# Kernel tuning notes

Hardware: AMD Instinct MI355X
Metric: run time of the kernel (lower is better)

Reference implementation:

```python
import jax, jax.numpy as jnp
import numpy as np

N, E, F_IN, H, K = 100000, 1600000, 256, 128, 5


def setup_inputs() -> dict:
    key = jax.random.key(0)
    ks = jax.random.split(key, 24)

    def rn(k, shape, scale=0.05):
        return jax.random.normal(k, shape, dtype=jnp.float32) * scale

    inp = {
        "x": rn(ks[0], (N, F_IN), 1.0),
        "edge_index": jax.random.randint(ks[1], (2, E), 0, N, dtype=jnp.int64),
        "edge_attr": jax.random.uniform(ks[2], (N, K), dtype=jnp.float32),
        "pre_W": rn(ks[3], (F_IN, H)),
        "pre_b": jnp.zeros((H,), jnp.float32),
        "c1_Ws": rn(ks[4], (H, H)),
        "c1_Wn": rn(ks[5], (H, H)),
        "c1_b": jnp.zeros((H,), jnp.float32),
        "c2_Ws": rn(ks[6], (H, H)),
        "c2_Wn": rn(ks[7], (H, H)),
        "c2_b": jnp.zeros((H,), jnp.float32),
        "nodepost_W": rn(ks[8], (H, H)),
        "nodepost_b": jnp.zeros((H,), jnp.float32),
        "d_W0": rn(ks[9], (K, H)),
        "d_b0": jnp.zeros((H,), jnp.float32),
        "d_W1": rn(ks[10], (H, H)),
        "d_b1": jnp.zeros((H,), jnp.float32),
        "d_W2": rn(ks[11], (H, H)),
        "d_b2": jnp.zeros((H,), jnp.float32),
        "d_W3": rn(ks[12], (H, H)),
        "d_b3": jnp.zeros((H,), jnp.float32),
        "final_W": rn(ks[13], (2 * H, 1)),
        "final_b": jnp.zeros((1,), jnp.float32),
    }
    return inp


def _mean_agg(h, src, dst, n):
    # scatter-mean of source features onto destination nodes
    s = jax.ops.segment_sum(h[src], dst, num_segments=n)  # [N, H]
    deg = jax.ops.segment_sum(jnp.ones_like(dst, dtype=h.dtype), dst, num_segments=n)
    return s / jnp.maximum(deg, 1.0)[:, None]


def reference(x, edge_index, edge_attr, pre_W, pre_b,
              c1_Ws, c1_Wn, c1_b, c2_Ws, c2_Wn, c2_b,
              nodepost_W, nodepost_b,
              d_W0, d_b0, d_W1, d_b1, d_W2, d_b2, d_W3, d_b3,
              final_W, final_b):
    n = x.shape[0]
    src, dst = edge_index[0], edge_index[1]

    # --- feat path: NodeAttributeAggregator ---
    h = x @ pre_W + pre_b                                   # pre_process_mlp
    agg = _mean_agg(h, src, dst, n)
    h = jax.nn.relu(h @ c1_Ws + agg @ c1_Wn + c1_b)          # layer1 conv + act
    agg = _mean_agg(h, src, dst, n)
    h = jax.nn.relu(h @ c2_Ws + agg @ c2_Wn + c2_b)          # layer2 conv + act
    feat_out = h @ nodepost_W + nodepost_b                   # post_process_mlp

    # --- dist path: EdgeAttributeAggregator (MLP over edge attrs) ---
    e = edge_attr.reshape(-1, K)
    y = jax.nn.relu(e @ d_W0 + d_b0)
    y = jax.nn.relu(y @ d_W1 + d_b1)
    y = jax.nn.relu(y @ d_W2 + d_b2)
    dist_out = y @ d_W3 + d_b3

    # --- merge 'cat' + final MLP + squeeze + sigmoid ---
    z = jnp.concatenate([feat_out, dist_out], axis=1)        # [N, 2H]
    out = (z @ final_W + final_b).squeeze(1)                  # [N]
    return jax.nn.sigmoid(out)
```

## Files before the change

kernel.cpp:

```cpp
#include <hip/hip_runtime.h>

#define HF 128
#define CAP 64
#define PSHIFT 17
#define BUCKET_BLOCKS 2048

typedef __attribute__((ext_vector_type(8))) short s16x8;
typedef __attribute__((ext_vector_type(4))) float f32x4;
typedef __attribute__((ext_vector_type(2))) float f32x2;

__device__ __forceinline__ unsigned short f2bf(float f) {
    unsigned u = __float_as_uint(f);
    return (unsigned short)((u + 0x7fff + ((u >> 16) & 1)) >> 16);
}
__device__ __forceinline__ float bflo(unsigned u) { return __uint_as_float(u << 16); }
__device__ __forceinline__ float bfhi(unsigned u) { return __uint_as_float(u & 0xffff0000u); }

#if __has_builtin(__builtin_amdgcn_cvt_pk_fp8_f32) && __has_builtin(__builtin_amdgcn_cvt_pk_f32_fp8)
#define FP8_HW 1
#else
#define FP8_HW 0
#endif

__device__ __forceinline__ unsigned char f2fp8(float f) {
#if FP8_HW
    int v = __builtin_amdgcn_cvt_pk_fp8_f32(f, f, 0, false);
    return (unsigned char)(v & 0xff);
#else
    unsigned u = __float_as_uint(f);
    unsigned s = (u >> 24) & 0x80;
    float a = fabsf(f);
    if (a > 448.f) a = 448.f;
    if (a < 0.015625f) {
        int q = (int)(a * 512.f + 0.5f);
        return (unsigned char)(s | q);
    }
    unsigned ub = __float_as_uint(a);
    ub += 0x0007ffff + ((ub >> 20) & 1);
    int e8 = (int)(ub >> 23) - 127 + 7;
    if (e8 >= 16) return (unsigned char)(s | 0x7e);
    return (unsigned char)(s | (e8 << 3) | ((ub >> 20) & 7));
#endif
}

__device__ __forceinline__ void fp8acc4(unsigned w, float* acc) {
#if FP8_HW
    f32x2 lo = __builtin_amdgcn_cvt_pk_f32_fp8(w, false);
    f32x2 hi = __builtin_amdgcn_cvt_pk_f32_fp8(w, true);
    acc[0] += lo.x; acc[1] += lo.y; acc[2] += hi.x; acc[3] += hi.y;
#else
    #pragma unroll
    for (int j = 0; j < 4; ++j) {
        unsigned b = (w >> (8 * j)) & 0xff;
        unsigned s = (b >> 7) & 1, e = (b >> 3) & 15, m = b & 7;
        float v = e ? __uint_as_float(((e + 120) << 23) | (m << 20))
                    : (float)m * 0.001953125f;
        acc[j] += s ? -v : v;
    }
#endif
}

__device__ __forceinline__ void repack_one(
    const float* __restrict__ W, short* __restrict__ Wp, int K, int t)
{
    int nkt = K >> 5;
    int lane = t & 63;
    int kt = (t >> 6) % nkt;
    int nt = (t >> 6) / nkt;
    int c = nt * 16 + (lane & 15);
    int kbase = kt * 32 + (lane >> 4) * 8;
    s16x8 v;
    #pragma unroll
    for (int j = 0; j < 8; ++j) v[j] = (short)f2bf(W[(long)(kbase + j) * HF + c]);
    *(s16x8*)(Wp + (long)t * 8) = v;
}

__global__ __launch_bounds__(256) void repack_all(
    const float* __restrict__ preW, const float* __restrict__ c1Ws,
    const float* __restrict__ c1Wn, const float* __restrict__ c2Ws,
    const float* __restrict__ c2Wn, const float* __restrict__ dW1,
    const float* __restrict__ dW2,
    short* preWp, short* c1Wsp, short* c1Wnp, short* c2Wsp, short* c2Wnp,
    short* dW1p, short* dW2p,
    const float* __restrict__ npW, const float* __restrict__ npb,
    const float* __restrict__ dW3, const float* __restrict__ db3,
    const float* __restrict__ fW,  const float* __restrict__ fb,
    float* __restrict__ uvc)
{
    int b = blockIdx.x;
    if (b == 64) {
        int i = threadIdx.x;
        if (i < HF) {
            float u = 0.f, v = 0.f;
            for (int j = 0; j < HF; ++j) {
                u += npW[i * HF + j] * fW[j];
                v += dW3[i * HF + j] * fW[HF + j];
            }
            uvc[i] = u;
            uvc[HF + i] = v;
            if (i == 0) {
                float c = fb[0];
                for (int j = 0; j < HF; ++j) c += npb[j] * fW[j] + db3[j] * fW[HF + j];
                uvc[2 * HF] = c;
            }
        }
        return;
    }
    if (b < 16) { repack_one(preW, preWp, 256, b * 256 + threadIdx.x); return; }
    int m = (b - 16) >> 3, t = ((b - 16) & 7) * 256 + threadIdx.x;
    const float* W; short* Wp;
    switch (m) {
        case 0: W = c1Ws; Wp = c1Wsp; break;
        case 1: W = c1Wn; Wp = c1Wnp; break;
        case 2: W = c2Ws; Wp = c2Wsp; break;
        case 3: W = c2Wn; Wp = c2Wnp; break;
        case 4: W = dW1;  Wp = dW1p;  break;
        default: W = dW2; Wp = dW2p;  break;
    }
    repack_one(W, Wp, HF, t);
}

__global__ __launch_bounds__(256) void bucketx_kernel(
    const int* __restrict__ eidx, long E,
    int* __restrict__ deg, int* __restrict__ bucket, int npass)
{
    const int xcd   = blockIdx.x & 7;
    const int chunk = blockIdx.x >> 3;
    const int nchunks = BUCKET_BLOCKS / 8;
    long per = (E + nchunks - 1) / nchunks;
    per = (per + 3) & ~3L;
    const long e0 = (long)chunk * per;
    const long e1 = (e0 + per < E) ? e0 + per : E;
    if (e0 >= E) return;
    for (int p = 0; p < npass; ++p) {
        for (long e = e0 + (long)threadIdx.x * 4; e + 4 <= e1; e += 1024) {
            int4 d4 = *(const int4*)(eidx + E + e);
            #pragma unroll
            for (int j = 0; j < 4; ++j) {
                int d = (&d4.x)[j];
                if ((d >> PSHIFT) != p || ((d >> 4) & 7) != xcd) continue;
                int s = eidx[e + j];
                int pos = atomicAdd(&deg[d], 1);
                if (pos < CAP) bucket[(long)d * CAP + pos] = s;
            }
        }
        for (long e = (e1 & ~3L) + threadIdx.x; e < e1; e += 256) {
            int d = eidx[E + e];
            if ((d >> PSHIFT) != p || ((d >> 4) & 7) != xcd) continue;
            int s = eidx[e];
            int pos = atomicAdd(&deg[d], 1);
            if (pos < CAP) bucket[(long)d * CAP + pos] = s;
        }
    }
}

__device__ __forceinline__ void agg_tile512(
    const unsigned char* __restrict__ hq, const int* __restrict__ deg,
    const int* __restrict__ bucket, int n, long row0B, int wv, int lane,
    unsigned* lds)
{
    const int g = lane >> 4;
    const int i = lane & 15;
    #pragma unroll
    for (int it = 0; it < 2; ++it) {
        const int rl = wv * 8 + it * 4 + g;
        const long node = row0B + rl;
        float acc[8];
        #pragma unroll
        for (int j = 0; j < 8; ++j) acc[j] = 0.f;
        int dg = 0, m = 0;
        const int* bl = bucket;
        if (node < n) {
            dg = deg[node];
            m = dg < CAP ? dg : CAP;
            bl = bucket + node * CAP;
        }
        int e = 0;
        for (; e + 8 <= m; e += 8) {
            int4 sa = *(const int4*)(bl + e);
            int4 sb = *(const int4*)(bl + e + 4);
            uint2 v0 = *(const uint2*)(hq + (long)sa.x * HF + i * 8);
            uint2 v1 = *(const uint2*)(hq + (long)sa.y * HF + i * 8);
            uint2 v2 = *(const uint2*)(hq + (long)sa.z * HF + i * 8);
            uint2 v3 = *(const uint2*)(hq + (long)sa.w * HF + i * 8);
            uint2 v4 = *(const uint2*)(hq + (long)sb.x * HF + i * 8);
            uint2 v5 = *(const uint2*)(hq + (long)sb.y * HF + i * 8);
            uint2 v6 = *(const uint2*)(hq + (long)sb.z * HF + i * 8);
            uint2 v7 = *(const uint2*)(hq + (long)sb.w * HF + i * 8);
            fp8acc4(v0.x, acc); fp8acc4(v0.y, acc + 4);
            fp8acc4(v1.x, acc); fp8acc4(v1.y, acc + 4);
            fp8acc4(v2.x, acc); fp8acc4(v2.y, acc + 4);
            fp8acc4(v3.x, acc); fp8acc4(v3.y, acc + 4);
            fp8acc4(v4.x, acc); fp8acc4(v4.y, acc + 4);
            fp8acc4(v5.x, acc); fp8acc4(v5.y, acc + 4);
            fp8acc4(v6.x, acc); fp8acc4(v6.y, acc + 4);
            fp8acc4(v7.x, acc); fp8acc4(v7.y, acc + 4);
        }
        for (; e + 4 <= m; e += 4) {
            int4 sa = *(const int4*)(bl + e);
            uint2 v0 = *(const uint2*)(hq + (long)sa.x * HF + i * 8);
            uint2 v1 = *(const uint2*)(hq + (long)sa.y * HF + i * 8);
            uint2 v2 = *(const uint2*)(hq + (long)sa.z * HF + i * 8);
            uint2 v3 = *(const uint2*)(hq + (long)sa.w * HF + i * 8);
            fp8acc4(v0.x, acc); fp8acc4(v0.y, acc + 4);
            fp8acc4(v1.x, acc); fp8acc4(v1.y, acc + 4);
            fp8acc4(v2.x, acc); fp8acc4(v2.y, acc + 4);
            fp8acc4(v3.x, acc); fp8acc4(v3.y, acc + 4);
        }
        for (; e < m; ++e) {
            uint2 v = *(const uint2*)(hq + (long)bl[e] * HF + i * 8);
            fp8acc4(v.x, acc); fp8acc4(v.y, acc + 4);
        }
        const float sc = 1.f / (float)(dg > 1 ? dg : 1);
        uint4 o;
        o.x = (unsigned)f2bf(acc[0] * sc) | ((unsigned)f2bf(acc[1] * sc) << 16);
        o.y = (unsigned)f2bf(acc[2] * sc) | ((unsigned)f2bf(acc[3] * sc) << 16);
        o.z = (unsigned)f2bf(acc[4] * sc) | ((unsigned)f2bf(acc[5] * sc) << 16);
        o.w = (unsigned)f2bf(acc[6] * sc) | ((unsigned)f2bf(acc[7] * sc) << 16);
        *(uint4*)&lds[rl * 64 + ((i ^ (rl & 15)) << 2)] = o;
    }
}

template<int K, bool F32>
__device__ __forceinline__ void gemm_pass_mfma(
    const void* __restrict__ Av, const short* __restrict__ Wp,
    long rA, int lane, f32x4 acc[8])
{
    const int q = lane >> 4;
    constexpr int NKT = K >> 5;
    #pragma unroll
    for (int kt = 0; kt < NKT; ++kt) {
        s16x8 a;
        if (F32) {
            const float* p = (const float*)Av + rA * K + kt * 32 + q * 8;
            float4 f0 = *(const float4*)p;
            float4 f1 = *(const float4*)(p + 4);
            a[0] = (short)f2bf(f0.x); a[1] = (short)f2bf(f0.y);
            a[2] = (short)f2bf(f0.z); a[3] = (short)f2bf(f0.w);
            a[4] = (short)f2bf(f1.x); a[5] = (short)f2bf(f1.y);
            a[6] = (short)f2bf(f1.z); a[7] = (short)f2bf(f1.w);
        } else {
            a = *(const s16x8*)((const unsigned short*)Av + rA * K + kt * 32 + q * 8);
        }
        #pragma unroll
        for (int nt = 0; nt < 8; ++nt) {
            s16x8 b = *(const s16x8*)(Wp + ((long)(nt * NKT + kt) * 64 + lane) * 8);
            acc[nt] = __builtin_amdgcn_mfma_f32_16x16x32_bf16(a, b, acc[nt], 0, 0, 0);
        }
    }
}

__device__ __forceinline__ void gemm_pass_lds(
    const unsigned* lds, int w, int lane, const short* __restrict__ Wp, f32x4 acc[8])
{
    const int q = lane >> 4;
    const int i15 = lane & 15;
    const int rl = w * 16 + i15;
    #pragma unroll
    for (int kt = 0; kt < 4; ++kt) {
        s16x8 a = *(const s16x8*)&lds[rl * 64 + (((kt * 4 + q) ^ i15) << 2)];
        #pragma unroll
        for (int nt = 0; nt < 8; ++nt) {
            s16x8 b = *(const s16x8*)(Wp + ((long)(nt * 4 + kt) * 64 + lane) * 8);
            acc[nt] = __builtin_amdgcn_mfma_f32_16x16x32_bf16(a, b, acc[nt], 0, 0, 0);
        }
    }
}

__device__ void pre_body(int gb, const float* __restrict__ x, const short* __restrict__ preWp,
                         const float* __restrict__ preb, unsigned short* __restrict__ h0,
                         unsigned char* __restrict__ h0q, int n)
{
    const int lane = threadIdx.x & 63;
    const int wv   = threadIdx.x >> 6;
    const long row0 = (long)gb * 64 + wv * 16;

    f32x4 acc[8];
    #pragma unroll
    for (int nt = 0; nt < 8; ++nt)
        #pragma unroll
        for (int i = 0; i < 4; ++i) acc[nt][i] = 0.f;

    long rA = row0 + (lane & 15);
    if (rA > n - 1) rA = n - 1;

    gemm_pass_mfma<256, true>(x, preWp, rA, lane, acc);

    const int cq = lane >> 4;
    #pragma unroll
    for (int nt = 0; nt < 8; ++nt) {
        int col = nt * 16 + (lane & 15);
        float bs = preb[col];
        #pragma unroll
        for (int i = 0; i < 4; ++i) {
            long r = row0 + cq * 4 + i;
            if (r < n) {
                float o = acc[nt][i] + bs;
                h0[r * HF + col] = f2bf(o);
                h0q[r * HF + col] = f2fp8(o);
            }
        }
    }
}

__device__ void disthead_body(int gb,
    const float* __restrict__ ea, const float* __restrict__ W0,
    const float* __restrict__ b0, const short* __restrict__ W1p,
    const float* __restrict__ b1, unsigned short* __restrict__ y1, int n)
{
    const int lane = threadIdx.x & 63;
    const int wv   = threadIdx.x >> 6;
    const long row0 = (long)gb * 64 + wv * 16;
    const int q = lane >> 4;
    long rA = row0 + (lane & 15);
    if (rA > n - 1) rA = n - 1;

    float e0 = ea[rA * 5 + 0], e1 = ea[rA * 5 + 1], e2 = ea[rA * 5 + 2],
          e3 = ea[rA * 5 + 3], e4 = ea[rA * 5 + 4];

    f32x4 acc[8];
    #pragma unroll
    for (int nt = 0; nt < 8; ++nt)
        #pragma unroll
        for (int i = 0; i < 4; ++i) acc[nt][i] = 0.f;

    #pragma unroll
    for (int kt = 0; kt < 4; ++kt) {
        const int c = kt * 32 + q * 8;
        s16x8 a;
        #pragma unroll
        for (int h = 0; h < 2; ++h) {
            float4 w0 = *(const float4*)(W0 + 0 * HF + c + h * 4);
            float4 w1 = *(const float4*)(W0 + 1 * HF + c + h * 4);
            float4 w2 = *(const float4*)(W0 + 2 * HF + c + h * 4);
            float4 w3 = *(const float4*)(W0 + 3 * HF + c + h * 4);
            float4 w4 = *(const float4*)(W0 + 4 * HF + c + h * 4);
            float4 bb = *(const float4*)(b0 + c + h * 4);
            float z0 = fmaxf(bb.x + e0 * w0.x + e1 * w1.x + e2 * w2.x + e3 * w3.x + e4 * w4.x, 0.f);
            float z1 = fmaxf(bb.y + e0 * w0.y + e1 * w1.y + e2 * w2.y + e3 * w3.y + e4 * w4.y, 0.f);
            float z2 = fmaxf(bb.z + e0 * w0.z + e1 * w1.z + e2 * w2.z + e3 * w3.z + e4 * w4.z, 0.f);
            float z3 = fmaxf(bb.w + e0 * w0.w + e1 * w1.w + e2 * w2.w + e3 * w3.w + e4 * w4.w, 0.f);
            a[h * 4 + 0] = (short)f2bf(z0); a[h * 4 + 1] = (short)f2bf(z1);
            a[h * 4 + 2] = (short)f2bf(z2); a[h * 4 + 3] = (short)f2bf(z3);
        }
        #pragma unroll
        for (int nt = 0; nt < 8; ++nt) {
            s16x8 b = *(const s16x8*)(W1p + ((long)(nt * 4 + kt) * 64 + lane) * 8);
            acc[nt] = __builtin_amdgcn_mfma_f32_16x16x32_bf16(a, b, acc[nt], 0, 0, 0);
        }
    }

    const int cq = lane >> 4;
    #pragma unroll
    for (int nt = 0; nt < 8; ++nt) {
        int col = nt * 16 + (lane & 15);
        float bs = b1[col];
        #pragma unroll
        for (int i = 0; i < 4; ++i) {
            long r = row0 + cq * 4 + i;
            if (r < n) y1[r * HF + col] = f2bf(fmaxf(acc[nt][i] + bs, 0.f));
        }
    }
}

__global__ __launch_bounds__(256) void megapd_kernel(
    const float* __restrict__ x, const short* __restrict__ preWp,
    const float* __restrict__ preb, unsigned short* __restrict__ h0,
    unsigned char* __restrict__ h0q,
    const float* __restrict__ ea, const float* __restrict__ W0,
    const float* __restrict__ b0, const short* __restrict__ W1p,
    const float* __restrict__ b1, unsigned short* __restrict__ y1,
    int n, int gemmBlocks)
{
    if (blockIdx.x < gemmBlocks)
        pre_body(blockIdx.x, x, preWp, preb, h0, h0q, n);
    else
        disthead_body(blockIdx.x - gemmBlocks, ea, W0, b0, W1p, b1, y1, n);
}

__global__ __launch_bounds__(512) void c1f_kernel(
    const unsigned short* __restrict__ h0, const unsigned char* __restrict__ h0q,
    const int* __restrict__ deg, const int* __restrict__ bucket,
    const short* __restrict__ Wsp, const short* __restrict__ Wnp,
    const float* __restrict__ bias, unsigned short* __restrict__ out,
    unsigned char* __restrict__ outq, int n)
{
    __shared__ unsigned ldsagg[64 * 64];
    const int lane = threadIdx.x & 63;
    const int wv   = threadIdx.x >> 6;
    const long row0B = (long)blockIdx.x * 64;

    agg_tile512(h0q, deg, bucket, n, row0B, wv, lane, ldsagg);
    __syncthreads();

    if (wv >= 4) return;

    f32x4 acc[8];
    #pragma unroll
    for (int nt = 0; nt < 8; ++nt)
        #pragma unroll
        for (int i = 0; i < 4; ++i) acc[nt][i] = 0.f;

    const long row0 = row0B + wv * 16;
    long rA = row0 + (lane & 15);
    if (rA > n - 1) rA = n - 1;

    gemm_pass_mfma<HF, false>((const void*)h0, Wsp, rA, lane, acc);
    gemm_pass_lds(ldsagg, wv, lane, Wnp, acc);

    const int cq = lane >> 4;
    #pragma unroll
    for (int nt = 0; nt < 8; ++nt) {
        int col = nt * 16 + (lane & 15);
        float bs = bias[col];
        #pragma unroll
        for (int i = 0; i < 4; ++i) {
            long r = row0 + cq * 4 + i;
            if (r < n) {
                float o = fmaxf(acc[nt][i] + bs, 0.f);
                out[r * HF + col] = f2bf(o);
                outq[r * HF + col] = f2fp8(o);
            }
        }
    }
}

__global__ __launch_bounds__(512) void tailf_kernel(
    const unsigned short* __restrict__ h1, const unsigned char* __restrict__ h1q,
    const unsigned short* __restrict__ y1,
    const int* __restrict__ deg, const int* __restrict__ bucket,
    const short* __restrict__ c2Wsp, const short* __restrict__ c2Wnp,
    const short* __restrict__ dW2p,
    const float* __restrict__ c2b, const float* __restrict__ db2,
    const float* __restrict__ uvc, float* __restrict__ out, int n)
{
    __shared__ unsigned ldsagg[64 * 64];
    __shared__ float pp[2][64];
    const int lane = threadIdx.x & 63;
    const int wv   = threadIdx.x >> 6;
    const long row0B = (long)blockIdx.x * 64;

    agg_tile512(h1q, deg, bucket, n, row0B, wv, lane, ldsagg);
    __syncthreads();

    const int w = wv & 3;
    const long row0 = row0B + w * 16;
    long rA = row0 + (lane & 15);
    if (rA > n - 1) rA = n - 1;
    const int cq = lane >> 4;
    float part[4] = {0.f, 0.f, 0.f, 0.f};

    f32x4 acc[8];
    #pragma unroll
    for (int nt = 0; nt < 8; ++nt)
        #pragma unroll
        for (int i = 0; i < 4; ++i) acc[nt][i] = 0.f;

    if (wv < 4) {
        gemm_pass_mfma<HF, false>((const void*)h1, c2Wsp, rA, lane, acc);
        gemm_pass_lds(ldsagg, w, lane, c2Wnp, acc);
        #pragma unroll
        for (int nt = 0; nt < 8; ++nt) {
            int col = nt * 16 + (lane & 15);
            float bh = c2b[col], uu = uvc[col];
            #pragma unroll
            for (int i = 0; i < 4; ++i)
                part[i] += fmaxf(acc[nt][i] + bh, 0.f) * uu;
        }
    } else {
        gemm_pass_mfma<HF, false>((const void*)y1, dW2p, rA, lane, acc);
        #pragma unroll
        for (int nt = 0; nt < 8; ++nt) {
            int col = nt * 16 + (lane & 15);
            float by = db2[col], vv = uvc[HF + col];
            #pragma unroll
            for (int i = 0; i < 4; ++i)
                part[i] += fmaxf(acc[nt][i] + by, 0.f) * vv;
        }
    }

    #pragma unroll
    for (int i = 0; i < 4; ++i) {
        float s = part[i];
        s += __shfl_xor(s, 1, 64);
        s += __shfl_xor(s, 2, 64);
        s += __shfl_xor(s, 4, 64);
        s += __shfl_xor(s, 8, 64);
        part[i] = s;
    }
    if ((lane & 15) == 0) {
        #pragma unroll
        for (int i = 0; i < 4; ++i)
            pp[wv >> 2][w * 16 + cq * 4 + i] = part[i];
    }
    __syncthreads();

    if (threadIdx.x < 64) {
        long r = row0B + threadIdx.x;
        if (r < n) {
            float s = pp[0][threadIdx.x] + pp[1][threadIdx.x] + uvc[2 * HF];
            out[r] = 1.f / (1.f + expf(-s));
        }
    }
}

extern "C" void kernel_launch(void* const* d_in, const int* in_sizes, int n_in,
                              void* d_out, int out_size, void* d_ws, size_t ws_size,
                              hipStream_t stream)
{
    const float* x      = (const float*)d_in[0];
    const int*   eidx   = (const int*)  d_in[1];
    const float* eattr  = (const float*)d_in[2];
    const float* pre_W  = (const float*)d_in[3];
    const float* pre_b  = (const float*)d_in[4];
    const float* c1_Ws  = (const float*)d_in[5];
    const float* c1_Wn  = (const float*)d_in[6];
    const float* c1_b   = (const float*)d_in[7];
    const float* c2_Ws  = (const float*)d_in[8];
    const float* c2_Wn  = (const float*)d_in[9];
    const float* c2_b   = (const float*)d_in[10];
    const float* npW    = (const float*)d_in[11];
    const float* npb    = (const float*)d_in[12];
    const float* dW0    = (const float*)d_in[13];
    const float* db0    = (const float*)d_in[14];
    const float* dW1    = (const float*)d_in[15];
    const float* db1    = (const float*)d_in[16];
    const float* dW2    = (const float*)d_in[17];
    const float* db2    = (const float*)d_in[18];
    const float* dW3    = (const float*)d_in[19];
    const float* db3    = (const float*)d_in[20];
    const float* fW     = (const float*)d_in[21];
    const float* fb     = (const float*)d_in[22];

    const int  n = in_sizes[0] / 256;
    const long E = in_sizes[1] / 2;

    char* ws = (char*)d_ws;
    size_t off = 0;
    auto alloc = [&](size_t bytes) -> void* {
        void* p = ws + off;
        off += (bytes + 255) & ~(size_t)255;
        return p;
    };
    unsigned short* B0 = (unsigned short*)alloc((size_t)n * HF * 2);
    unsigned short* B1 = (unsigned short*)alloc((size_t)n * HF * 2);
    unsigned short* B2 = (unsigned short*)alloc((size_t)n * HF * 2);
    unsigned char*  B0q = (unsigned char*)alloc((size_t)n * HF);
    unsigned char*  B1q = (unsigned char*)alloc((size_t)n * HF);
    int*   deg    = (int*)alloc((size_t)n * sizeof(int));
    int*   bucket = (int*)alloc((size_t)n * CAP * sizeof(int));
    float* uvc    = (float*)alloc((2 * HF + 1) * sizeof(float));
    short* preWp  = (short*)alloc(256 * HF * 2);
    short* c1Wsp  = (short*)alloc(HF * HF * 2);
    short* c1Wnp  = (short*)alloc(HF * HF * 2);
    short* c2Wsp  = (short*)alloc(HF * HF * 2);
    short* c2Wnp  = (short*)alloc(HF * HF * 2);
    short* dW1p   = (short*)alloc(HF * HF * 2);
    short* dW2p   = (short*)alloc(HF * HF * 2);

    const int gemmBlocks = (n + 63) / 64;
    const int npass = ((n - 1) >> PSHIFT) + 1;

    repack_all<<<65, 256, 0, stream>>>(
        pre_W, c1_Ws, c1_Wn, c2_Ws, c2_Wn, dW1, dW2,
        preWp, c1Wsp, c1Wnp, c2Wsp, c2Wnp, dW1p, dW2p,
        npW, npb, dW3, db3, fW, fb, uvc);

    hipMemsetAsync(deg, 0, (size_t)n * sizeof(int), stream);

    bucketx_kernel<<<BUCKET_BLOCKS, 256, 0, stream>>>(eidx, E, deg, bucket, npass);

    megapd_kernel<<<2 * gemmBlocks, 256, 0, stream>>>(
        x, preWp, pre_b, B0, B0q,
        eattr, dW0, db0, dW1p, db1, B2,
        n, gemmBlocks);

    c1f_kernel<<<gemmBlocks, 512, 0, stream>>>(
        B0, B0q, deg, bucket, c1Wsp, c1Wnp, c1_b, B1, B1q, n);

    tailf_kernel<<<gemmBlocks, 512, 0, stream>>>(
        B1, B1q, B2, deg, bucket, c2Wsp, c2Wnp, dW2p, c2_b, db2, uvc, (float*)d_out, n);
}
```

Measured before the change: 330.3 us.

## Split GEMM output columns across 8 waves and stage x tile in LDS

```diff
diff --git a/kernel.cpp b/kernel.cpp
--- a/kernel.cpp
+++ b/kernel.cpp
@@ -13,8 +13,6 @@
     unsigned u = __float_as_uint(f);
     return (unsigned short)((u + 0x7fff + ((u >> 16) & 1)) >> 16);
 }
-__device__ __forceinline__ float bflo(unsigned u) { return __uint_as_float(u << 16); }
-__device__ __forceinline__ float bfhi(unsigned u) { return __uint_as_float(u & 0xffff0000u); }
 
 #if __has_builtin(__builtin_amdgcn_cvt_pk_fp8_f32) && __has_builtin(__builtin_amdgcn_cvt_pk_f32_fp8)
 #define FP8_HW 1
@@ -221,44 +219,48 @@
     }
 }
 
-template<int K, bool F32>
-__device__ __forceinline__ void gemm_pass_mfma(
-    const void* __restrict__ Av, const short* __restrict__ Wp,
-    long rA, int lane, f32x4 acc[8])
+__device__ __forceinline__ void gemm_pass4(
+    const unsigned short* __restrict__ Av, const short* __restrict__ Wp,
+    long rA, int lane, int nb, f32x4 acc[4])
 {
     const int q = lane >> 4;
-    constexpr int NKT = K >> 5;
-    #pragma unroll
-    for (int kt = 0; kt < NKT; ++kt) {
-        s16x8 a;
-        if (F32) {
-            const float* p = (const float*)Av + rA * K + kt * 32 + q * 8;
-            float4 f0 = *(const float4*)p;
-            float4 f1 = *(const float4*)(p + 4);
-            a[0] = (short)f2bf(f0.x); a[1] = (short)f2bf(f0.y);
-            a[2] = (short)f2bf(f0.z); a[3] = (short)f2bf(f0.w);
-            a[4] = (short)f2bf(f1.x); a[5] = (short)f2bf(f1.y);
-            a[6] = (short)f2bf(f1.z); a[7] = (short)f2bf(f1.w);
-        } else {
-            a = *(const s16x8*)((const unsigned short*)Av + rA * K + kt * 32 + q * 8);
-        }
-        #pragma unroll
-        for (int nt = 0; nt < 8; ++nt) {
-            s16x8 b = *(const s16x8*)(Wp + ((long)(nt * NKT + kt) * 64 + lane) * 8);
-            acc[nt] = __builtin_amdgcn_mfma_f32_16x16x32_bf16(a, b, acc[nt], 0, 0, 0);
-        }
-    }
-}
-
-__device__ __forceinline__ void gemm_pass_lds(
-    const unsigned* lds, int w, int lane, const short* __restrict__ Wp, f32x4 acc[8])
+    #pragma unroll
+    for (int kt = 0; kt < 4; ++kt) {
+        s16x8 a = *(const s16x8*)(Av + rA * HF + kt * 32 + q * 8);
+        #pragma unroll
+        for (int j = 0; j < 4; ++j) {
+            s16x8 b = *(const s16x8*)(Wp + ((long)((nb + j) * 4 + kt) * 64 + lane) * 8);
+            acc[j] = __builtin_amdgcn_mfma_f32_16x16x32_bf16(a, b, acc[j], 0, 0, 0);
+        }
+    }
+}
+
+__device__ __forceinline__ void gemm_pass_lds4(
+    const unsigned* lds, int w3, int lane, const short* __restrict__ Wp,
+    int nb, f32x4 acc[4])
 {
     const int q = lane >> 4;
     const int i15 = lane & 15;
-    const int rl = w * 16 + i15;
+    const int rl = w3 * 16 + i15;
     #pragma unroll
     for (int kt = 0; kt < 4; ++kt) {
         s16x8 a = *(const s16x8*)&lds[rl * 64 + (((kt * 4 + q) ^ i15) << 2)];
+        #pragma unroll
+        for (int j = 0; j < 4; ++j) {
+            s16x8 b = *(const s16x8*)(Wp + ((long)((nb + j) * 4 + kt) * 64 + lane) * 8);
+            acc[j] = __builtin_amdgcn_mfma_f32_16x16x32_bf16(a, b, acc[j], 0, 0, 0);
+        }
+    }
+}
+
+__device__ __forceinline__ void gemm_pass_mfma8(
+    const unsigned short* __restrict__ Av, const short* __restrict__ Wp,
+    long rA, int lane, f32x4 acc[8])
+{
+    const int q = lane >> 4;
+    #pragma unroll
+    for (int kt = 0; kt < 4; ++kt) {
+        s16x8 a = *(const s16x8*)(Av + rA * HF + kt * 32 + q * 8);
         #pragma unroll
         for (int nt = 0; nt < 8; ++nt) {
             s16x8 b = *(const s16x8*)(Wp + ((long)(nt * 4 + kt) * 64 + lane) * 8);
@@ -267,103 +269,24 @@
     }
 }
 
-__device__ void pre_body(int gb, const float* __restrict__ x, const short* __restrict__ preWp,
-                         const float* __restrict__ preb, unsigned short* __restrict__ h0,
-                         unsigned char* __restrict__ h0q, int n)
-{
-    const int lane = threadIdx.x & 63;
-    const int wv   = threadIdx.x >> 6;
-    const long row0 = (long)gb * 64 + wv * 16;
-
-    f32x4 acc[8];
-    #pragma unroll
-    for (int nt = 0; nt < 8; ++nt)
-        #pragma unroll
-        for (int i = 0; i < 4; ++i) acc[nt][i] = 0.f;
-
-    long rA = row0 + (lane & 15);
-    if (rA > n - 1) rA = n - 1;
-
-    gemm_pass_mfma<256, true>(x, preWp, rA, lane, acc);
-
-    const int cq = lane >> 4;
-    #pragma unroll
-    for (int nt = 0; nt < 8; ++nt) {
-        int col = nt * 16 + (lane & 15);
-        float bs = preb[col];
-        #pragma unroll
-        for (int i = 0; i < 4; ++i) {
-            long r = row0 + cq * 4 + i;
-            if (r < n) {
-                float o = acc[nt][i] + bs;
-                h0[r * HF + col] = f2bf(o);
-                h0q[r * HF + col] = f2fp8(o);
-            }
-        }
-    }
-}
-
-__device__ void disthead_body(int gb,
-    const float* __restrict__ ea, const float* __restrict__ W0,
-    const float* __restrict__ b0, const short* __restrict__ W1p,
-    const float* __restrict__ b1, unsigned short* __restrict__ y1, int n)
-{
-    const int lane = threadIdx.x & 63;
-    const int wv   = threadIdx.x >> 6;
-    const long row0 = (long)gb * 64 + wv * 16;
+__device__ __forceinline__ void gemm_pass_lds8(
+    const unsigned* lds, int w3, int lane, const short* __restrict__ Wp, f32x4 acc[8])
+{
     const int q = lane >> 4;
-    long rA = row0 + (lane & 15);
-    if (rA > n - 1) rA = n - 1;
-
-    float e0 = ea[rA * 5 + 0], e1 = ea[rA * 5 + 1], e2 = ea[rA * 5 + 2],
-          e3 = ea[rA * 5 + 3], e4 = ea[rA * 5 + 4];
-
-    f32x4 acc[8];
-    #pragma unroll
-    for (int nt = 0; nt < 8; ++nt)
-        #pragma unroll
-        for (int i = 0; i < 4; ++i) acc[nt][i] = 0.f;
-
+    const int i15 = lane & 15;
+    const int rl = w3 * 16 + i15;
     #pragma unroll
     for (int kt = 0; kt < 4; ++kt) {
-        const int c = kt * 32 + q * 8;
-        s16x8 a;
-        #pragma unroll
-        for (int h = 0; h < 2; ++h) {
-            float4 w0 = *(const float4*)(W0 + 0 * HF + c + h * 4);
-            float4 w1 = *(const float4*)(W0 + 1 * HF + c + h * 4);
-            float4 w2 = *(const float4*)(W0 + 2 * HF + c + h * 4);
-            float4 w3 = *(const float4*)(W0 + 3 * HF + c + h * 4);
-            float4 w4 = *(const float4*)(W0 + 4 * HF + c + h * 4);
-            float4 bb = *(const float4*)(b0 + c + h * 4);
-            float z0 = fmaxf(bb.x + e0 * w0.x + e1 * w1.x + e2 * w2.x + e3 * w3.x + e4 * w4.x, 0.f);
-            float z1 = fmaxf(bb.y + e0 * w0.y + e1 * w1.y + e2 * w2.y + e3 * w3.y + e4 * w4.y, 0.f);
-            float z2 = fmaxf(bb.z + e0 * w0.z + e1 * w1.z + e2 * w2.z + e3 * w3.z + e4 * w4.z, 0.f);
-            float z3 = fmaxf(bb.w + e0 * w0.w + e1 * w1.w + e2 * w2.w + e3 * w3.w + e4 * w4.w, 0.f);
-            a[h * 4 + 0] = (short)f2bf(z0); a[h * 4 + 1] = (short)f2bf(z1);
-            a[h * 4 + 2] = (short)f2bf(z2); a[h * 4 + 3] = (short)f2bf(z3);
-        }
+        s16x8 a = *(const s16x8*)&lds[rl * 64 + (((kt * 4 + q) ^ i15) << 2)];
         #pragma unroll
         for (int nt = 0; nt < 8; ++nt) {
-            s16x8 b = *(const s16x8*)(W1p + ((long)(nt * 4 + kt) * 64 + lane) * 8);
+            s16x8 b = *(const s16x8*)(Wp + ((long)(nt * 4 + kt) * 64 + lane) * 8);
             acc[nt] = __builtin_amdgcn_mfma_f32_16x16x32_bf16(a, b, acc[nt], 0, 0, 0);
         }
     }
-
-    const int cq = lane >> 4;
-    #pragma unroll
-    for (int nt = 0; nt < 8; ++nt) {
-        int col = nt * 16 + (lane & 15);
-        float bs = b1[col];
-        #pragma unroll
-        for (int i = 0; i < 4; ++i) {
-            long r = row0 + cq * 4 + i;
-            if (r < n) y1[r * HF + col] = f2bf(fmaxf(acc[nt][i] + bs, 0.f));
-        }
-    }
-}
-
-__global__ __launch_bounds__(256) void megapd_kernel(
+}
+
+__global__ __launch_bounds__(512) void megapd_kernel(
     const float* __restrict__ x, const short* __restrict__ preWp,
     const float* __restrict__ preb, unsigned short* __restrict__ h0,
     unsigned char* __restrict__ h0q,
@@ -372,10 +295,126 @@
     const float* __restrict__ b1, unsigned short* __restrict__ y1,
     int n, int gemmBlocks)
 {
-    if (blockIdx.x < gemmBlocks)
-        pre_body(blockIdx.x, x, preWp, preb, h0, h0q, n);
-    else
-        disthead_body(blockIdx.x - gemmBlocks, ea, W0, b0, W1p, b1, y1, n);
+    __shared__ unsigned ldsx[64 * 128];
+    const int lane = threadIdx.x & 63;
+    const int wv   = threadIdx.x >> 6;
+    const int w3   = wv & 3;
+    const int nb   = (wv >> 2) * 4;
+
+    if (blockIdx.x < gemmBlocks) {
+        const long row0B = (long)blockIdx.x * 64;
+        {
+            const int t = threadIdx.x;
+            const int row = t >> 3;
+            const int c0 = (t & 7) * 32;
+            long rr = row0B + row;
+            if (rr > n - 1) rr = n - 1;
+            const float* xp = x + rr * 256 + c0;
+            unsigned pk[16];
+            #pragma unroll
+            for (int k = 0; k < 8; ++k) {
+                float4 f = *(const float4*)(xp + k * 4);
+                pk[2 * k]     = (unsigned)f2bf(f.x) | ((unsigned)f2bf(f.y) << 16);
+                pk[2 * k + 1] = (unsigned)f2bf(f.z) | ((unsigned)f2bf(f.w) << 16);
+            }
+            #pragma unroll
+            for (int k = 0; k < 4; ++k) {
+                int c = (t & 7) * 4 + k;
+                int phys = c ^ (row & 31);
+                *(uint4*)&ldsx[row * 128 + phys * 4] =
+                    make_uint4(pk[4 * k], pk[4 * k + 1], pk[4 * k + 2], pk[4 * k + 3]);
+            }
+        }
+        __syncthreads();
+
+        f32x4 acc[4];
+        #pragma unroll
+        for (int j = 0; j < 4; ++j)
+            #pragma unroll
+            for (int i = 0; i < 4; ++i) acc[j][i] = 0.f;
+
+        const int rl = w3 * 16 + (lane & 15);
+        const int q = lane >> 4;
+        #pragma unroll
+        for (int kt = 0; kt < 8; ++kt) {
+            int c = kt * 4 + q;
+            s16x8 a = *(const s16x8*)&ldsx[rl * 128 + ((c ^ (rl & 31)) << 2)];
+            #pragma unroll
+            for (int j = 0; j < 4; ++j) {
+                s16x8 b = *(const s16x8*)(preWp + ((long)((nb + j) * 8 + kt) * 64 + lane) * 8);
+                acc[j] = __builtin_amdgcn_mfma_f32_16x16x32_bf16(a, b, acc[j], 0, 0, 0);
+            }
+        }
+
+        const long row0 = row0B + w3 * 16;
+        const int cq = lane >> 4;
+        #pragma unroll
+        for (int j = 0; j < 4; ++j) {
+            int col = (nb + j) * 16 + (lane & 15);
+            float bs = preb[col];
+            #pragma unroll
+            for (int i = 0; i < 4; ++i) {
+                long r = row0 + cq * 4 + i;
+                if (r < n) {
+                    float o = acc[j][i] + bs;
+                    h0[r * HF + col] = f2bf(o);
+                    h0q[r * HF + col] = f2fp8(o);
+                }
+            }
+        }
+    } else {
+        const long row0 = (long)(blockIdx.x - gemmBlocks) * 64 + w3 * 16;
+        const int q = lane >> 4;
+        long rA = row0 + (lane & 15);
+        if (rA > n - 1) rA = n - 1;
+
+        float e0 = ea[rA * 5 + 0], e1 = ea[rA * 5 + 1], e2 = ea[rA * 5 + 2],
+              e3 = ea[rA * 5 + 3], e4 = ea[rA * 5 + 4];
+
+        f32x4 acc[4];
+        #pragma unroll
+        for (int j = 0; j < 4; ++j)
+            #pragma unroll
+            for (int i = 0; i < 4; ++i) acc[j][i] = 0.f;
+
+        #pragma unroll
+        for (int kt = 0; kt < 4; ++kt) {
+            const int c = kt * 32 + q * 8;
+            s16x8 a;
+            #pragma unroll
+            for (int h = 0; h < 2; ++h) {
+                float4 w0 = *(const float4*)(W0 + 0 * HF + c + h * 4);
+                float4 w1 = *(const float4*)(W0 + 1 * HF + c + h * 4);
+                float4 w2 = *(const float4*)(W0 + 2 * HF + c + h * 4);
+                float4 w3v = *(const float4*)(W0 + 3 * HF + c + h * 4);
+                float4 w4 = *(const float4*)(W0 + 4 * HF + c + h * 4);
+                float4 bb = *(const float4*)(b0 + c + h * 4);
+                float z0 = fmaxf(bb.x + e0 * w0.x + e1 * w1.x + e2 * w2.x + e3 * w3v.x + e4 * w4.x, 0.f);
+                float z1 = fmaxf(bb.y + e0 * w0.y + e1 * w1.y + e2 * w2.y + e3 * w3v.y + e4 * w4.y, 0.f);
+                float z2 = fmaxf(bb.z + e0 * w0.z + e1 * w1.z + e2 * w2.z + e3 * w3v.z + e4 * w4.z, 0.f);
+                float z3 = fmaxf(bb.w + e0 * w0.w + e1 * w1.w + e2 * w2.w + e3 * w3v.w + e4 * w4.w, 0.f);
+                a[h * 4 + 0] = (short)f2bf(z0); a[h * 4 + 1] = (short)f2bf(z1);
+                a[h * 4 + 2] = (short)f2bf(z2); a[h * 4 + 3] = (short)f2bf(z3);
+            }
+            #pragma unroll
+            for (int j = 0; j < 4; ++j) {
+                s16x8 b = *(const s16x8*)(W1p + ((long)((nb + j) * 4 + kt) * 64 + lane) * 8);
+                acc[j] = __builtin_amdgcn_mfma_f32_16x16x32_bf16(a, b, acc[j], 0, 0, 0);
+            }
+        }
+
+        const int cq = lane >> 4;
+        #pragma unroll
+        for (int j = 0; j < 4; ++j) {
+            int col = (nb + j) * 16 + (lane & 15);
+            float bs = b1[col];
+            #pragma unroll
+            for (int i = 0; i < 4; ++i) {
+                long r = row0 + cq * 4 + i;
+                if (r < n) y1[r * HF + col] = f2bf(fmaxf(acc[j][i] + bs, 0.f));
+            }
+        }
+    }
 }
 
 __global__ __launch_bounds__(512) void c1f_kernel(
@@ -393,31 +432,32 @@
     agg_tile512(h0q, deg, bucket, n, row0B, wv, lane, ldsagg);
     __syncthreads();
 
-    if (wv >= 4) return;
-
-    f32x4 acc[8];
-    #pragma unroll
-    for (int nt = 0; nt < 8; ++nt)
-        #pragma unroll
-        for (int i = 0; i < 4; ++i) acc[nt][i] = 0.f;
-
-    const long row0 = row0B + wv * 16;
+    const int w3 = wv & 3;
+    const int nb = (wv >> 2) * 4;
+
+    f32x4 acc[4];
+    #pragma unroll
+    for (int j = 0; j < 4; ++j)
+        #pragma unroll
+        for (int i = 0; i < 4; ++i) acc[j][i] = 0.f;
+
+    const long row0 = row0B + w3 * 16;
     long rA = row0 + (lane & 15);
     if (rA > n - 1) rA = n - 1;
 
-    gemm_pass_mfma<HF, false>((const void*)h0, Wsp, rA, lane, acc);
-    gemm_pass_lds(ldsagg, wv, lane, Wnp, acc);
+    gemm_pass4(h0, Wsp, rA, lane, nb, acc);
+    gemm_pass_lds4(ldsagg, w3, lane, Wnp, nb, acc);
 
     const int cq = lane >> 4;
     #pragma unroll
-    for (int nt = 0; nt < 8; ++nt) {
-        int col = nt * 16 + (lane & 15);
+    for (int j = 0; j < 4; ++j) {
+        int col = (nb + j) * 16 + (lane & 15);
         float bs = bias[col];
         #pragma unroll
         for (int i = 0; i < 4; ++i) {
             long r = row0 + cq * 4 + i;
             if (r < n) {
-                float o = fmaxf(acc[nt][i] + bs, 0.f);
+                float o = fmaxf(acc[j][i] + bs, 0.f);
                 out[r * HF + col] = f2bf(o);
                 outq[r * HF + col] = f2fp8(o);
             }
@@ -457,8 +497,8 @@
         for (int i = 0; i < 4; ++i) acc[nt][i] = 0.f;
 
     if (wv < 4) {
-        gemm_pass_mfma<HF, false>((const void*)h1, c2Wsp, rA, lane, acc);
-        gemm_pass_lds(ldsagg, w, lane, c2Wnp, acc);
+        gemm_pass_mfma8(h1, c2Wsp, rA, lane, acc);
+        gemm_pass_lds8(ldsagg, w, lane, c2Wnp, acc);
         #pragma unroll
         for (int nt = 0; nt < 8; ++nt) {
             int col = nt * 16 + (lane & 15);
@@ -468,7 +508,7 @@
                 part[i] += fmaxf(acc[nt][i] + bh, 0.f) * uu;
         }
     } else {
-        gemm_pass_mfma<HF, false>((const void*)y1, dW2p, rA, lane, acc);
+        gemm_pass_mfma8(y1, dW2p, rA, lane, acc);
         #pragma unroll
         for (int nt = 0; nt < 8; ++nt) {
             int col = nt * 16 + (lane & 15);
@@ -570,7 +610,7 @@
 
     bucketx_kernel<<<BUCKET_BLOCKS, 256, 0, stream>>>(eidx, E, deg, bucket, npass);
 
-    megapd_kernel<<<2 * gemmBlocks, 256, 0, stream>>>(
+    megapd_kernel<<<2 * gemmBlocks, 512, 0, stream>>>(
         x, preWp, pre_b, B0, B0q,
         eattr, dW0, db0, dW1p, db1, B2,
         n, gemmBlocks);
```

Result: faster. 316.1 us (-4.3%).
